# Kernel optimization log

Measured on AMD Instinct MI355X. Metric: run time of the kernel, lower is better.

## Reference

```python
import jax, jax.numpy as jnp
import numpy as np

K = 7          # kernel_size
PAD = 3        # (dilation*(K-1)+1)//2
EPS = 1e-5     # BatchNorm eps
B, CIN, H, W = 4, 256, 56, 56
CR = 32        # rel_planes
COUT = 256     # out_planes
SP = 8         # share_planes
HN = COUT // SP  # attention heads = 32
OFFS = [(dy, dx) for dy in range(K) for dx in range(K)]


def setup_inputs() -> dict:
    key = jax.random.key(0)
    ks = jax.random.split(key, 24)
    def n(i, shape, s=0.05):
        return jax.random.normal(ks[i], shape, dtype=jnp.float32) * s
    def pos(i, shape):  # positive values for BN gamma / running var
        return jax.random.uniform(ks[i], shape, dtype=jnp.float32, minval=0.5, maxval=1.5)
    return {
        "x": jax.random.normal(ks[0], (B, CIN, H, W), dtype=jnp.float32),
        "w1c": n(1, (CR, CIN)),  "b1c": n(2, (CR,)),
        "w2c": n(3, (CR, CIN)),  "b2c": n(4, (CR,)),
        "w3c": n(5, (COUT, CIN)), "b3c": n(6, (COUT,)),
        "bn1_g": pos(7, (CR,)), "bn1_b": n(8, (CR,)), "bn1_m": n(9, (CR,)), "bn1_v": pos(10, (CR,)),
        "cw1": n(11, (CR, CR)),
        "bn2_g": pos(12, (CR,)), "bn2_b": n(13, (CR,)), "bn2_m": n(14, (CR,)), "bn2_v": pos(15, (CR,)),
        "cw2": n(16, (HN, CR)), "cw2_b": n(17, (HN,)),
    }


def _conv1x1(x, w, b):
    # x: [B,C,H,W], w: [O,C]
    return jnp.einsum('bchw,oc->bohw', x, w) + b[None, :, None, None]


def _bn(y, g, b, m, v):
    # inference BatchNorm2d over channel axis 1; y is 4D
    inv = g / jnp.sqrt(v + EPS)
    return y * inv[None, :, None, None] + (b - m * inv)[None, :, None, None]


def reference(x, w1c, b1c, w2c, b2c, w3c, b3c,
              bn1_g, bn1_b, bn1_m, bn1_v, cw1,
              bn2_g, bn2_b, bn2_m, bn2_v, cw2, cw2_b):
    x1 = _conv1x1(x, w1c, b1c)   # [B,CR,H,W]  query
    x2 = _conv1x1(x, w2c, b2c)   # [B,CR,H,W]  key
    x3 = _conv1x1(x, w3c, b3c)   # [B,COUT,H,W] value

    # Subtraction2 with reflection padding (pad_mode=1):
    # diff[b,c,k,i] = x1[b,c,i] - patch_k(x2)[b,c,i]
    x2p = jnp.pad(x2, ((0, 0), (0, 0), (PAD, PAD), (PAD, PAD)), mode='reflect')
    diff = jnp.stack([x1 - x2p[:, :, dy:dy + H, dx:dx + W] for dy, dx in OFFS],
                     axis=2)                      # [B,CR,49,H,W]
    diff = diff.reshape(B, CR, K * K, H * W)      # [B,CR,49,HW]

    # conv_w: BN -> ReLU -> 1x1 conv (no bias) -> BN -> ReLU -> 1x1 conv
    y = jax.nn.relu(_bn(diff, bn1_g, bn1_b, bn1_m, bn1_v))
    y = jnp.einsum('bkln,ok->boln', y, cw1)       # [B,CR,49,HW]
    y = jax.nn.relu(_bn(y, bn2_g, bn2_b, bn2_m, bn2_v))
    logits = jnp.einsum('bkln,ok->boln', y, cw2) + cw2_b[None, :, None, None]
    wgt = jax.nn.softmax(logits, axis=2)          # softmax over k^2, [B,HN,49,HW]
    wgt = wgt.reshape(B, HN, K * K, H, W)

    # Aggregation with reflection padding: out[b,c,i] = sum_k patch_k(x3)[b,c,i] * w[b,c//SP,k,i]
    x3p = jnp.pad(x3, ((0, 0), (0, 0), (PAD, PAD), (PAD, PAD)), mode='reflect')
    out = jnp.zeros((B, HN, SP, H, W), dtype=x.dtype)
    for k, (dy, dx) in enumerate(OFFS):
        patch = x3p[:, :, dy:dy + H, dx:dx + W].reshape(B, HN, SP, H, W)
        out = out + patch * wgt[:, :, k][:, :, None]
    return out.reshape(B, COUT, H, W)
```

## Files before the change

kernel.cpp:

```cpp
#include <hip/hip_runtime.h>
#include <math.h>

#define HW_N   3136
#define W_DIM  56
#define C_IN   256
#define C_R    32
#define C_OUT  256
#define C_ALL  320
#define K2D    49
#define RS     40
#define BN_EPS 1e-5f

typedef _Float16 h2 __attribute__((ext_vector_type(2)));
typedef __fp16  g2 __attribute__((ext_vector_type(2)));
typedef __fp16  g4 __attribute__((ext_vector_type(4)));
typedef __fp16  g8 __attribute__((ext_vector_type(8)));
typedef float   f4 __attribute__((ext_vector_type(4)));

__device__ __forceinline__ h2 pkrtz(float a, float b) {
    g2 r = __builtin_amdgcn_cvt_pkrtz(a, b);
    return __builtin_bit_cast(h2, r);
}

__device__ __forceinline__ g8 pack8(float4 a, float4 b) {
    g2 p0 = __builtin_amdgcn_cvt_pkrtz(a.x, a.y);
    g2 p1 = __builtin_amdgcn_cvt_pkrtz(a.z, a.w);
    g2 p2 = __builtin_amdgcn_cvt_pkrtz(b.x, b.y);
    g2 p3 = __builtin_amdgcn_cvt_pkrtz(b.z, b.w);
    g8 o;
    o[0] = p0[0]; o[1] = p0[1]; o[2] = p1[0]; o[3] = p1[1];
    o[4] = p2[0]; o[5] = p2[1]; o[6] = p3[0]; o[7] = p3[1];
    return o;
}

__device__ __forceinline__ int refl(int v) {
    v = (v < 0) ? -v : v;
    return (v > 55) ? (110 - v) : v;
}

__device__ __forceinline__ void wave_fence() {
    asm volatile("s_waitcnt lgkmcnt(0)" ::: "memory");
}

__global__ __launch_bounds__(256) void k_prep_w(
    const float* __restrict__ w1c, const float* __restrict__ w2c,
    const float* __restrict__ w3c, __fp16* __restrict__ wh)
{
    const int idx = blockIdx.x * 256 + threadIdx.x;
    const int r  = idx >> 6;
    const int c4 = (idx & 63) * 4;
    const float* wp = (r < 32) ? (w1c + r * C_IN)
                    : (r < 64) ? (w2c + (r - 32) * C_IN)
                               : (w3c + (r - 64) * C_IN);
    const float4 wv = *(const float4*)(wp + c4);
    const g2 lo = __builtin_amdgcn_cvt_pkrtz(wv.x, wv.y);
    const g2 hi = __builtin_amdgcn_cvt_pkrtz(wv.z, wv.w);
    g4 o; o[0] = lo[0]; o[1] = lo[1]; o[2] = hi[0]; o[3] = hi[1];
    *(g4*)(wh + (size_t)r * C_IN + c4) = o;
}

__global__ __launch_bounds__(256) void k_prep_x(
    const float* __restrict__ x, __fp16* __restrict__ xT16)
{
    const int t   = threadIdx.x;
    const int b   = blockIdx.z;
    const int pos = blockIdx.x * 64 + (t & 63);
    const int ci0 = (blockIdx.y * 4 + (t >> 6)) * 32;
    const float* __restrict__ xp = x + ((size_t)b * C_IN + ci0) * HW_N + pos;
    float v[32];
#pragma unroll
    for (int j = 0; j < 32; ++j) v[j] = xp[(size_t)j * HW_N];
    __fp16* op = xT16 + ((size_t)b * HW_N + pos) * C_IN + ci0;
#pragma unroll
    for (int q = 0; q < 4; ++q) {
        g8 o;
#pragma unroll
        for (int i = 0; i < 4; ++i) {
            const g2 p = __builtin_amdgcn_cvt_pkrtz(v[q * 8 + 2 * i], v[q * 8 + 2 * i + 1]);
            o[2 * i] = p[0]; o[2 * i + 1] = p[1];
        }
        *(g8*)(op + q * 8) = o;
    }
}

__global__ __launch_bounds__(256) void k_conv_mfma(
    const __fp16* __restrict__ xT16, const __fp16* __restrict__ wh,
    const float* __restrict__ b1c, const float* __restrict__ b2c,
    const float* __restrict__ b3c, float* __restrict__ xall)
{
    const int t = threadIdx.x, w = t >> 6, lane = t & 63;
    const int quad = lane >> 4, l16 = lane & 15;
    const int b = blockIdx.z, pos0 = blockIdx.x * 64, co0 = blockIdx.y * 64;
    const int co_row = co0 + w * 16 + l16;

    const __fp16* arow = xT16 + ((size_t)b * HW_N + pos0 + l16) * C_IN + quad * 8;
    const __fp16* brow = wh + (size_t)co_row * C_IN + quad * 8;

    f4 acc[4];
#pragma unroll
    for (int mt = 0; mt < 4; ++mt) acc[mt] = (f4){0.f, 0.f, 0.f, 0.f};

#pragma unroll
    for (int ks = 0; ks < 8; ++ks) {
        const g8 bf = *(const g8*)(brow + ks * 32);
#pragma unroll
        for (int mt = 0; mt < 4; ++mt) {
            const g8 af = *(const g8*)(arow + (size_t)mt * 16 * C_IN + ks * 32);
            acc[mt] = __builtin_amdgcn_mfma_f32_16x16x32_f16(af, bf, acc[mt], 0, 0, 0);
        }
    }

    const float bias = (co_row < 32) ? b1c[co_row]
                     : (co_row < 64) ? b2c[co_row - 32] : b3c[co_row - 64];
#pragma unroll
    for (int mt = 0; mt < 4; ++mt) {
#pragma unroll
        for (int r = 0; r < 4; ++r) {
            const int pos_w = pos0 + mt * 16 + quad * 4 + r;
            xall[((size_t)b * HW_N + pos_w) * C_ALL + co_row] = acc[mt][r] + bias;
        }
    }
}

__global__ __launch_bounds__(256) void k_attn(
    const float* __restrict__ xall,
    const float* __restrict__ bn1_g, const float* __restrict__ bn1_b,
    const float* __restrict__ bn1_m, const float* __restrict__ bn1_v,
    const float* __restrict__ cw1,
    const float* __restrict__ bn2_g, const float* __restrict__ bn2_b,
    const float* __restrict__ bn2_m, const float* __restrict__ bn2_v,
    const float* __restrict__ cw2, const float* __restrict__ cw2_b,
    float* __restrict__ outt)
{
    __shared__ __align__(16) _Float16 tbuf[4][64 * RS];
    __shared__ int pk[4][52];
    const int tid = threadIdx.x;
    const int w = tid >> 6, lane = tid & 63;
    const int b = blockIdx.y;
    const int bid  = blockIdx.x;
    const int posb = (bid & 7) * 98 + (bid >> 3);
    const int pos  = posb * 4 + w;
    const int y0 = pos / W_DIM, x0 = pos - y0 * W_DIM;
    const float* __restrict__ base = xall + (size_t)b * HW_N * C_ALL;
    _Float16* tb = tbuf[w];

    {
        const int c2 = lane & 15;
        const int kh = lane >> 4;
        const float2 g = *(const float2*)(bn1_g + 2 * c2);
        const float2 bb = *(const float2*)(bn1_b + 2 * c2);
        const float2 m = *(const float2*)(bn1_m + 2 * c2);
        const float2 v = *(const float2*)(bn1_v + 2 * c2);
        const float iv0 = g.x * rsqrtf(v.x + BN_EPS), bt0 = bb.x - m.x * iv0;
        const float iv1 = g.y * rsqrtf(v.y + BN_EPS), bt1 = bb.y - m.y * iv1;
        const float2 x1v = *(const float2*)(base + (size_t)pos * C_ALL + 2 * c2);
#pragma unroll
        for (int j = 0; j < 13; ++j) {
            const int k = 4 * j + kh;
            if (k < K2D) {
                const int dy = k / 7, dx = k - dy * 7;
                const int rp = refl(y0 + dy - 3) * W_DIM + refl(x0 + dx - 3);
                if (c2 == 0) pk[w][k] = rp;
                const float2 x2v = *(const float2*)(base + (size_t)rp * C_ALL + 32 + 2 * c2);
                const float t0 = fmaxf((x1v.x - x2v.x) * iv0 + bt0, 0.f);
                const float t1 = fmaxf((x1v.y - x2v.y) * iv1 + bt1, 0.f);
                *(h2*)&tb[k * RS + 2 * c2] = pkrtz(t0, t1);
            }
        }
    }
    wave_fence();

    const int quad = lane >> 4, l16 = lane & 15;
    f4 acc[4][2];

    {
        g8 bf[2];
#pragma unroll
        for (int nt = 0; nt < 2; ++nt) {
            const float* wr = cw1 + (nt * 16 + l16) * C_R + quad * 8;
            bf[nt] = pack8(*(const float4*)wr, *(const float4*)(wr + 4));
        }
#pragma unroll
        for (int mt = 0; mt < 4; ++mt) {
            acc[mt][0] = (f4){0.f, 0.f, 0.f, 0.f};
            acc[mt][1] = (f4){0.f, 0.f, 0.f, 0.f};
            const g8 af = *(const g8*)((const __fp16*)tb + (mt * 16 + l16) * RS + quad * 8);
            acc[mt][0] = __builtin_amdgcn_mfma_f32_16x16x32_f16(af, bf[0], acc[mt][0], 0, 0, 0);
            acc[mt][1] = __builtin_amdgcn_mfma_f32_16x16x32_f16(af, bf[1], acc[mt][1], 0, 0, 0);
        }
    }
    wave_fence();

#pragma unroll
    for (int nt = 0; nt < 2; ++nt) {
        const int o = nt * 16 + l16;
        const float iv = bn2_g[o] * rsqrtf(bn2_v[o] + BN_EPS);
        const float bt = bn2_b[o] - bn2_m[o] * iv;
#pragma unroll
        for (int mt = 0; mt < 4; ++mt)
#pragma unroll
            for (int r = 0; r < 4; ++r) {
                const int row = mt * 16 + quad * 4 + r;
                tb[row * RS + o] = (_Float16)fmaxf(acc[mt][nt][r] * iv + bt, 0.f);
            }
    }
    wave_fence();

    {
        g8 bf[2];
#pragma unroll
        for (int nt = 0; nt < 2; ++nt) {
            const float* wr = cw2 + (nt * 16 + l16) * C_R + quad * 8;
            bf[nt] = pack8(*(const float4*)wr, *(const float4*)(wr + 4));
        }
#pragma unroll
        for (int mt = 0; mt < 4; ++mt) {
            acc[mt][0] = (f4){0.f, 0.f, 0.f, 0.f};
            acc[mt][1] = (f4){0.f, 0.f, 0.f, 0.f};
            const g8 af = *(const g8*)((const __fp16*)tb + (mt * 16 + l16) * RS + quad * 8);
            acc[mt][0] = __builtin_amdgcn_mfma_f32_16x16x32_f16(af, bf[0], acc[mt][0], 0, 0, 0);
            acc[mt][1] = __builtin_amdgcn_mfma_f32_16x16x32_f16(af, bf[1], acc[mt][1], 0, 0, 0);
        }
    }
    wave_fence();

#pragma unroll
    for (int nt = 0; nt < 2; ++nt) {
        const float bsv = cw2_b[nt * 16 + l16];
        float m = -1e30f;
#pragma unroll
        for (int mt = 0; mt < 4; ++mt)
#pragma unroll
            for (int r = 0; r < 4; ++r) {
                const int k = mt * 16 + quad * 4 + r;
                const float v = acc[mt][nt][r] + bsv;
                acc[mt][nt][r] = v;
                if (k < K2D) m = fmaxf(m, v);
            }
        m = fmaxf(m, __shfl_xor(m, 16, 64));
        m = fmaxf(m, __shfl_xor(m, 32, 64));
        float s = 0.f;
#pragma unroll
        for (int mt = 0; mt < 4; ++mt)
#pragma unroll
            for (int r = 0; r < 4; ++r) {
                const int k = mt * 16 + quad * 4 + r;
                const float e = (k < K2D) ? __expf(acc[mt][nt][r] - m) : 0.f;
                acc[mt][nt][r] = e;
                s += e;
            }
        s += __shfl_xor(s, 16, 64);
        s += __shfl_xor(s, 32, 64);
        const float rs = 1.f / s;
        const int o = nt * 16 + l16;
#pragma unroll
        for (int mt = 0; mt < 4; ++mt)
#pragma unroll
            for (int r = 0; r < 4; ++r) {
                const int row = mt * 16 + quad * 4 + r;
                tb[row * RS + o] = (_Float16)(acc[mt][nt][r] * rs);
            }
    }
    wave_fence();

    {
        const int hn = lane >> 1;
        float4 a = make_float4(0.f, 0.f, 0.f, 0.f);
#pragma unroll 7
        for (int k = 0; k < K2D; ++k) {
            const int rp = pk[w][k];
            const float wv = (float)tb[k * RS + hn];
            const float4 v = *(const float4*)(base + (size_t)rp * C_ALL + 64 + lane * 4);
            a.x += v.x * wv; a.y += v.y * wv; a.z += v.z * wv; a.w += v.w * wv;
        }
        *(float4*)(outt + ((size_t)b * HW_N + pos) * C_OUT + lane * 4) = a;
    }
}

__global__ __launch_bounds__(256) void k_transpose(
    const float* __restrict__ in, float* __restrict__ out)
{
    __shared__ float ts[32][33];
    const int tid = threadIdx.x;
    const int b  = blockIdx.z;
    const int i0 = blockIdx.x * 32;
    const int c0 = blockIdx.y * 32;
    const int rr = tid >> 5, cc = tid & 31;
#pragma unroll
    for (int r = 0; r < 4; ++r) {
        const int ii = rr * 4 + r;
        ts[ii][cc] = in[((size_t)b * HW_N + i0 + ii) * C_OUT + c0 + cc];
    }
    __syncthreads();
#pragma unroll
    for (int r = 0; r < 4; ++r) {
        const int ccl = rr * 4 + r;
        out[((size_t)b * C_OUT + c0 + ccl) * HW_N + i0 + cc] = ts[cc][ccl];
    }
}

extern "C" void kernel_launch(void* const* d_in, const int* in_sizes, int n_in,
                              void* d_out, int out_size, void* d_ws, size_t ws_size,
                              hipStream_t stream)
{
    const float* x     = (const float*)d_in[0];
    const float* w1c   = (const float*)d_in[1];
    const float* b1c   = (const float*)d_in[2];
    const float* w2c   = (const float*)d_in[3];
    const float* b2c   = (const float*)d_in[4];
    const float* w3c   = (const float*)d_in[5];
    const float* b3c   = (const float*)d_in[6];
    const float* bn1_g = (const float*)d_in[7];
    const float* bn1_b = (const float*)d_in[8];
    const float* bn1_m = (const float*)d_in[9];
    const float* bn1_v = (const float*)d_in[10];
    const float* cw1   = (const float*)d_in[11];
    const float* bn2_g = (const float*)d_in[12];
    const float* bn2_b = (const float*)d_in[13];
    const float* bn2_m = (const float*)d_in[14];
    const float* bn2_v = (const float*)d_in[15];
    const float* cw2   = (const float*)d_in[16];
    const float* cw2_b = (const float*)d_in[17];

    float* xall = (float*)d_ws;
    float* outt = xall + (size_t)4 * HW_N * C_ALL;
    __fp16* xT16 = (__fp16*)outt;
    __fp16* wh   = xT16 + (size_t)4 * HW_N * C_IN;

    k_prep_w<<<80, 256, 0, stream>>>(w1c, w2c, w3c, wh);
    k_prep_x<<<dim3(49, 2, 4), 256, 0, stream>>>(x, xT16);
    k_conv_mfma<<<dim3(49, 5, 4), 256, 0, stream>>>(xT16, wh, b1c, b2c, b3c, xall);
    k_attn<<<dim3(784, 4, 1), 256, 0, stream>>>(xall,
        bn1_g, bn1_b, bn1_m, bn1_v, cw1,
        bn2_g, bn2_b, bn2_m, bn2_v, cw2, cw2_b, outt);
    k_transpose<<<dim3(98, 8, 4), 256, 0, stream>>>(outt, (float*)d_out);
}
```

Baseline: 169.3 us.

## Store conv outputs as fp16, fuse weight prep and output transpose into neighbours

The 1x1 conv now converts fp32 weights to fp16 on the fly, so the separate weight-prep kernel is gone. Its result goes through shared memory and is written as packed fp16, which halves the intermediate buffer read by the attention kernel. The attention kernel stages the four per-pixel outputs of each block in shared memory and writes straight to the NCHW output with float4 stores, so the separate transpose kernel and its extra round trip are removed. This cuts two launches and a large share of global traffic. The cost is a precision loss in the stored q/k/v values and strided 16-byte output writes.

```diff
diff --git a/kernel.cpp b/kernel.cpp
--- a/kernel.cpp
+++ b/kernel.cpp
@@ -42,23 +42,6 @@
     asm volatile("s_waitcnt lgkmcnt(0)" ::: "memory");
 }
 
-__global__ __launch_bounds__(256) void k_prep_w(
-    const float* __restrict__ w1c, const float* __restrict__ w2c,
-    const float* __restrict__ w3c, __fp16* __restrict__ wh)
-{
-    const int idx = blockIdx.x * 256 + threadIdx.x;
-    const int r  = idx >> 6;
-    const int c4 = (idx & 63) * 4;
-    const float* wp = (r < 32) ? (w1c + r * C_IN)
-                    : (r < 64) ? (w2c + (r - 32) * C_IN)
-                               : (w3c + (r - 64) * C_IN);
-    const float4 wv = *(const float4*)(wp + c4);
-    const g2 lo = __builtin_amdgcn_cvt_pkrtz(wv.x, wv.y);
-    const g2 hi = __builtin_amdgcn_cvt_pkrtz(wv.z, wv.w);
-    g4 o; o[0] = lo[0]; o[1] = lo[1]; o[2] = hi[0]; o[3] = hi[1];
-    *(g4*)(wh + (size_t)r * C_IN + c4) = o;
-}
-
 __global__ __launch_bounds__(256) void k_prep_x(
     const float* __restrict__ x, __fp16* __restrict__ xT16)
 {
@@ -84,17 +67,26 @@
 }
 
 __global__ __launch_bounds__(256) void k_conv_mfma(
-    const __fp16* __restrict__ xT16, const __fp16* __restrict__ wh,
+    const __fp16* __restrict__ xT16,
+    const float* __restrict__ w1c, const float* __restrict__ w2c,
+    const float* __restrict__ w3c,
     const float* __restrict__ b1c, const float* __restrict__ b2c,
-    const float* __restrict__ b3c, float* __restrict__ xall)
+    const float* __restrict__ b3c, __fp16* __restrict__ xall16)
 {
+    __shared__ __align__(16) float cs[64][68];
     const int t = threadIdx.x, w = t >> 6, lane = t & 63;
     const int quad = lane >> 4, l16 = lane & 15;
     const int b = blockIdx.z, pos0 = blockIdx.x * 64, co0 = blockIdx.y * 64;
     const int co_row = co0 + w * 16 + l16;
 
+    const float* wp = (co_row < 32) ? (w1c + co_row * C_IN)
+                    : (co_row < 64) ? (w2c + (co_row - 32) * C_IN)
+                                    : (w3c + (co_row - 64) * C_IN);
+    const float bias = (co_row < 32) ? b1c[co_row]
+                     : (co_row < 64) ? b2c[co_row - 32] : b3c[co_row - 64];
+
     const __fp16* arow = xT16 + ((size_t)b * HW_N + pos0 + l16) * C_IN + quad * 8;
-    const __fp16* brow = wh + (size_t)co_row * C_IN + quad * 8;
+    const float* brow = wp + quad * 8;
 
     f4 acc[4];
 #pragma unroll
@@ -102,7 +94,8 @@
 
 #pragma unroll
     for (int ks = 0; ks < 8; ++ks) {
-        const g8 bf = *(const g8*)(brow + ks * 32);
+        const g8 bf = pack8(*(const float4*)(brow + ks * 32),
+                            *(const float4*)(brow + ks * 32 + 4));
 #pragma unroll
         for (int mt = 0; mt < 4; ++mt) {
             const g8 af = *(const g8*)(arow + (size_t)mt * 16 * C_IN + ks * 32);
@@ -110,38 +103,45 @@
         }
     }
 
-    const float bias = (co_row < 32) ? b1c[co_row]
-                     : (co_row < 64) ? b2c[co_row - 32] : b3c[co_row - 64];
-#pragma unroll
-    for (int mt = 0; mt < 4; ++mt) {
-#pragma unroll
-        for (int r = 0; r < 4; ++r) {
-            const int pos_w = pos0 + mt * 16 + quad * 4 + r;
-            xall[((size_t)b * HW_N + pos_w) * C_ALL + co_row] = acc[mt][r] + bias;
-        }
-    }
+#pragma unroll
+    for (int mt = 0; mt < 4; ++mt)
+#pragma unroll
+        for (int r = 0; r < 4; ++r)
+            cs[mt * 16 + quad * 4 + r][w * 16 + l16] = acc[mt][r] + bias;
+    __syncthreads();
+
+    const int pr = t >> 2, cq = (t & 3) * 16;
+    const float4 v0 = *(const float4*)&cs[pr][cq];
+    const float4 v1 = *(const float4*)&cs[pr][cq + 4];
+    const float4 v2 = *(const float4*)&cs[pr][cq + 8];
+    const float4 v3 = *(const float4*)&cs[pr][cq + 12];
+    __fp16* op = xall16 + ((size_t)b * HW_N + pos0 + pr) * C_ALL + co0 + cq;
+    *(g8*)op = pack8(v0, v1);
+    *(g8*)(op + 8) = pack8(v2, v3);
 }
 
 __global__ __launch_bounds__(256) void k_attn(
-    const float* __restrict__ xall,
+    const __fp16* __restrict__ xq,
     const float* __restrict__ bn1_g, const float* __restrict__ bn1_b,
     const float* __restrict__ bn1_m, const float* __restrict__ bn1_v,
     const float* __restrict__ cw1,
     const float* __restrict__ bn2_g, const float* __restrict__ bn2_b,
     const float* __restrict__ bn2_m, const float* __restrict__ bn2_v,
     const float* __restrict__ cw2, const float* __restrict__ cw2_b,
-    float* __restrict__ outt)
+    float* __restrict__ out)
 {
     __shared__ __align__(16) _Float16 tbuf[4][64 * RS];
+    __shared__ __align__(16) float stage[4][256];
     __shared__ int pk[4][52];
     const int tid = threadIdx.x;
     const int w = tid >> 6, lane = tid & 63;
     const int b = blockIdx.y;
     const int bid  = blockIdx.x;
     const int posb = (bid & 7) * 98 + (bid >> 3);
-    const int pos  = posb * 4 + w;
+    const int pos0 = posb * 4;
+    const int pos  = pos0 + w;
     const int y0 = pos / W_DIM, x0 = pos - y0 * W_DIM;
-    const float* __restrict__ base = xall + (size_t)b * HW_N * C_ALL;
+    const __fp16* __restrict__ base16 = xq + (size_t)b * HW_N * C_ALL;
     _Float16* tb = tbuf[w];
 
     {
@@ -153,7 +153,8 @@
         const float2 v = *(const float2*)(bn1_v + 2 * c2);
         const float iv0 = g.x * rsqrtf(v.x + BN_EPS), bt0 = bb.x - m.x * iv0;
         const float iv1 = g.y * rsqrtf(v.y + BN_EPS), bt1 = bb.y - m.y * iv1;
-        const float2 x1v = *(const float2*)(base + (size_t)pos * C_ALL + 2 * c2);
+        const g2 x1p = *(const g2*)(base16 + (size_t)pos * C_ALL + 2 * c2);
+        const float x1a = (float)x1p[0], x1b = (float)x1p[1];
 #pragma unroll
         for (int j = 0; j < 13; ++j) {
             const int k = 4 * j + kh;
@@ -161,9 +162,9 @@
                 const int dy = k / 7, dx = k - dy * 7;
                 const int rp = refl(y0 + dy - 3) * W_DIM + refl(x0 + dx - 3);
                 if (c2 == 0) pk[w][k] = rp;
-                const float2 x2v = *(const float2*)(base + (size_t)rp * C_ALL + 32 + 2 * c2);
-                const float t0 = fmaxf((x1v.x - x2v.x) * iv0 + bt0, 0.f);
-                const float t1 = fmaxf((x1v.y - x2v.y) * iv1 + bt1, 0.f);
+                const g2 x2p = *(const g2*)(base16 + (size_t)rp * C_ALL + 32 + 2 * c2);
+                const float t0 = fmaxf((x1a - (float)x2p[0]) * iv0 + bt0, 0.f);
+                const float t1 = fmaxf((x1b - (float)x2p[1]) * iv1 + bt1, 0.f);
                 *(h2*)&tb[k * RS + 2 * c2] = pkrtz(t0, t1);
             }
         }
@@ -270,32 +271,20 @@
         for (int k = 0; k < K2D; ++k) {
             const int rp = pk[w][k];
             const float wv = (float)tb[k * RS + hn];
-            const float4 v = *(const float4*)(base + (size_t)rp * C_ALL + 64 + lane * 4);
-            a.x += v.x * wv; a.y += v.y * wv; a.z += v.z * wv; a.w += v.w * wv;
-        }
-        *(float4*)(outt + ((size_t)b * HW_N + pos) * C_OUT + lane * 4) = a;
-    }
-}
-
-__global__ __launch_bounds__(256) void k_transpose(
-    const float* __restrict__ in, float* __restrict__ out)
-{
-    __shared__ float ts[32][33];
-    const int tid = threadIdx.x;
-    const int b  = blockIdx.z;
-    const int i0 = blockIdx.x * 32;
-    const int c0 = blockIdx.y * 32;
-    const int rr = tid >> 5, cc = tid & 31;
-#pragma unroll
-    for (int r = 0; r < 4; ++r) {
-        const int ii = rr * 4 + r;
-        ts[ii][cc] = in[((size_t)b * HW_N + i0 + ii) * C_OUT + c0 + cc];
+            const g4 v = *(const g4*)(base16 + (size_t)rp * C_ALL + 64 + lane * 4);
+            a.x += (float)v[0] * wv; a.y += (float)v[1] * wv;
+            a.z += (float)v[2] * wv; a.w += (float)v[3] * wv;
+        }
+        *(float4*)&stage[w][lane * 4] = a;
     }
     __syncthreads();
-#pragma unroll
-    for (int r = 0; r < 4; ++r) {
-        const int ccl = rr * 4 + r;
-        out[((size_t)b * C_OUT + c0 + ccl) * HW_N + i0 + cc] = ts[cc][ccl];
+
+    {
+        const int c = tid;
+        float4 o;
+        o.x = stage[0][c]; o.y = stage[1][c];
+        o.z = stage[2][c]; o.w = stage[3][c];
+        *(float4*)(out + ((size_t)b * C_OUT + c) * HW_N + pos0) = o;
     }
 }
 
@@ -322,16 +311,13 @@
     const float* cw2   = (const float*)d_in[16];
     const float* cw2_b = (const float*)d_in[17];
 
-    float* xall = (float*)d_ws;
-    float* outt = xall + (size_t)4 * HW_N * C_ALL;
-    __fp16* xT16 = (__fp16*)outt;
-    __fp16* wh   = xT16 + (size_t)4 * HW_N * C_IN;
-
-    k_prep_w<<<80, 256, 0, stream>>>(w1c, w2c, w3c, wh);
+    __fp16* xT16   = (__fp16*)d_ws;
+    __fp16* xall16 = xT16 + (size_t)4 * HW_N * C_IN;
+
     k_prep_x<<<dim3(49, 2, 4), 256, 0, stream>>>(x, xT16);
-    k_conv_mfma<<<dim3(49, 5, 4), 256, 0, stream>>>(xT16, wh, b1c, b2c, b3c, xall);
-    k_attn<<<dim3(784, 4, 1), 256, 0, stream>>>(xall,
+    k_conv_mfma<<<dim3(49, 5, 4), 256, 0, stream>>>(xT16, w1c, w2c, w3c,
+                                                    b1c, b2c, b3c, xall16);
+    k_attn<<<dim3(784, 4, 1), 256, 0, stream>>>(xall16,
         bn1_g, bn1_b, bn1_m, bn1_v, cw1,
-        bn2_g, bn2_b, bn2_m, bn2_v, cw2, cw2_b, outt);
-    k_transpose<<<dim3(98, 8, 4), 256, 0, stream>>>(outt, (float*)d_out);
-}
+        bn2_g, bn2_b, bn2_m, bn2_v, cw2, cw2_b, (float*)d_out);
+}
```

After: 167.7 us. About the same (-0.9%).
